# Kernel tuning notes

Measured on AMD Instinct MI355X. Metric: run time of the kernel, lower is better.

Reference implementation:

```python
import jax, jax.numpy as jnp
import numpy as np

H = 128; B = 128; NA = 32; N = B * NA; NH = 4; DH = H // NH; F = 2 * H + 3


def _ln(x, g, b, eps=1e-5):
    m = x.mean(-1, keepdims=True)
    v = ((x - m) ** 2).mean(-1, keepdims=True)
    return (x - m) / jnp.sqrt(v + eps) * g + b


def _silu(x):
    return x * jax.nn.sigmoid(x)


def setup_inputs() -> dict:
    key = jax.random.key(0)
    ks = jax.random.split(key, 16)
    def rn(i, shape, s=0.05):
        return jax.random.normal(ks[i], shape, jnp.float32) * s
    return dict(
        num_atoms=jnp.full((B,), NA, dtype=jnp.int32),
        elems=jax.random.randint(ks[0], (N,), 0, 119),
        cell=jnp.tile(10.0 * jnp.eye(3, dtype=jnp.float32), (B, 1)),  # [3B,3]
        coord=jax.random.uniform(ks[1], (N, 3), jnp.float32, 1.0, 9.0),
        emb=rn(2, (119, H), 1.0),
        ln_in_g=jnp.ones((H,), jnp.float32), ln_in_b=jnp.zeros((H,), jnp.float32),
        attn_in_w=rn(3, (H, 3 * H)), attn_in_b=jnp.zeros((3 * H,), jnp.float32),
        attn_out_w=rn(4, (H, H)), attn_out_b=jnp.zeros((H,), jnp.float32),
        ce_w1=rn(5, (3, H)), ce_b1=jnp.zeros((H,), jnp.float32),
        ce_w2=rn(6, (H, H)), ce_b2=jnp.zeros((H,), jnp.float32),
        ln_feat_g=jnp.ones((F,), jnp.float32), ln_feat_b=jnp.zeros((F,), jnp.float32),
        op_w1=rn(7, (F, H)), op_b1=jnp.zeros((H,), jnp.float32),
        op_ln1_g=jnp.ones((H,), jnp.float32), op_ln1_b=jnp.zeros((H,), jnp.float32),
        res_w1=rn(8, (H, H)), res_b1=jnp.zeros((H,), jnp.float32),
        res_ln_g=jnp.ones((H,), jnp.float32), res_ln_b=jnp.zeros((H,), jnp.float32),
        res_w2=rn(9, (H, H)), res_b2=jnp.zeros((H,), jnp.float32),
        op_ln2_g=jnp.ones((H,), jnp.float32), op_ln2_b=jnp.zeros((H,), jnp.float32),
        op_w3=rn(10, (H, 3)), op_b3=jnp.zeros((3,), jnp.float32),
    )


def reference(num_atoms, elems, cell, coord, emb, ln_in_g, ln_in_b,
              attn_in_w, attn_in_b, attn_out_w, attn_out_b,
              ce_w1, ce_b1, ce_w2, ce_b2, ln_feat_g, ln_feat_b,
              op_w1, op_b1, op_ln1_g, op_ln1_b,
              res_w1, res_b1, res_ln_g, res_ln_b, res_w2, res_b2,
              op_ln2_g, op_ln2_b, op_w3, op_b3):
    n = coord.shape[0]
    # atom embedding + input LayerNorm
    x = _ln(emb[elems], ln_in_g, ln_in_b)
    # unbatched multihead self-attention over all atoms (seq_len = n)
    qkv = x @ attn_in_w + attn_in_b
    q, k, v = jnp.split(qkv, 3, axis=-1)
    q = q.reshape(n, NH, DH); k = k.reshape(n, NH, DH); v = v.reshape(n, NH, DH)
    a = jax.nn.softmax(jnp.einsum('qhd,khd->hqk', q, k) / np.float32(np.sqrt(DH)), axis=-1)
    x = jnp.einsum('hqk,khd->qhd', a, v).reshape(n, H) @ attn_out_w + attn_out_b
    # cell encoder on [3B,3] rows
    cf = _silu(cell @ ce_w1 + ce_b1) @ ce_w2 + ce_b2
    bidx = jnp.repeat(jnp.arange(num_atoms.shape[0]), num_atoms, total_repeat_length=n)
    # torch: cf.repeat(B,1)[batch_idx] == cf[batch_idx] since batch_idx < B
    comb = _ln(jnp.concatenate([x, cf[bidx], coord], axis=-1), ln_feat_g, ln_feat_b)
    # offset predictor
    h = _silu(_ln(comb @ op_w1 + op_b1, op_ln1_g, op_ln1_b))
    h = h + (_silu(_ln(h @ res_w1 + res_b1, res_ln_g, res_ln_b)) @ res_w2 + res_b2)
    h = _ln(h, op_ln2_g, op_ln2_b)
    offset = jnp.tanh(h @ op_w3 + op_b3) * 0.01
    perturbed = coord + offset
    # per-molecule clamp: segment gather of per-cell-row min/max replaces the python loop
    c3 = cell.reshape(-1, 3, 3)           # [B,3,3]
    cmin = c3.min(axis=2) + 1e-6          # [B,3]
    cmax = c3.max(axis=2) - 1e-6          # [B,3]
    return jnp.clip(perturbed, cmin[bidx], cmax[bidx])
```

## Files before the change

### kernel.cpp

```cpp
#include <hip/hip_runtime.h>
#include <hip/hip_bf16.h>
#include <math.h>
#include <stdint.h>

#define NATOMS 4096
#define HD     128
#define NHEAD  4
#define DHEAD  32
#define FDIM   259
#define BATCH  128
#define H3X    384
#define SPLIT  4

typedef __attribute__((ext_vector_type(8))) short short8;
typedef __attribute__((ext_vector_type(4))) float float4v;
typedef __attribute__((ext_vector_type(16))) float f32x16;

__device__ __forceinline__ ushort f2bf(float f) {
    uint32_t u = __float_as_uint(f);
    return (ushort)((u + 0x7fffu + ((u >> 16) & 1u)) >> 16);
}
__device__ __forceinline__ float b2f(ushort u) {
    return __uint_as_float(((uint32_t)u) << 16);
}
__device__ __forceinline__ f32x16 z16() {
    f32x16 v;
#pragma unroll
    for (int i = 0; i < 16; i++) v[i] = 0.f;
    return v;
}

#define NB_PACK 528
#define NB_CELL 128
__global__ __launch_bounds__(256) void k_setup(
        const int* __restrict__ num_atoms, const float* __restrict__ cell,
        const float* __restrict__ qkvw, const float* __restrict__ aow,
        const float* __restrict__ op1w, const float* __restrict__ r1w,
        const float* __restrict__ r2w,
        const float* __restrict__ ce_w1, const float* __restrict__ ce_b1,
        const float* __restrict__ ce_w2, const float* __restrict__ ce_b2,
        int* __restrict__ bidx, float* __restrict__ cmin, float* __restrict__ cmax,
        ushort* __restrict__ Wqkv, ushort* __restrict__ Wao,
        ushort* __restrict__ Wop1, ushort* __restrict__ Wr1, ushort* __restrict__ Wr2,
        float* __restrict__ CF) {
    __shared__ float hs[HD];
    __shared__ int start[BATCH + 1];
    const int t = threadIdx.x;
    if (blockIdx.x < NB_PACK) {
        int idx = blockIdx.x * 256 + t;
        if (idx < 49152) {
            int n = idx >> 7, k = idx & 127;
            Wqkv[idx] = f2bf(qkvw[k * H3X + n]);
        } else if (idx < 65536) {
            int j = idx - 49152; int n = j >> 7, k = j & 127;
            Wao[j] = f2bf(aow[k * HD + n]);
        } else if (idx < 102400) {
            int j = idx - 65536; int n = j / 288, k = j - n * 288;
            Wop1[j] = (k < FDIM) ? f2bf(op1w[k * HD + n]) : (ushort)0;
        } else if (idx < 118784) {
            int j = idx - 102400; int n = j >> 7, k = j & 127;
            Wr1[j] = f2bf(r1w[k * HD + n]);
        } else if (idx < 135168) {
            int j = idx - 118784; int n = j >> 7, k = j & 127;
            Wr2[j] = f2bf(r2w[k * HD + n]);
        }
    } else if (blockIdx.x < NB_PACK + NB_CELL) {
        int r = blockIdx.x - NB_PACK;
        if (t < 128) {
            float c0 = cell[r * 3 + 0], c1 = cell[r * 3 + 1], c2 = cell[r * 3 + 2];
            float h = c0 * ce_w1[t] + c1 * ce_w1[HD + t] + c2 * ce_w1[2 * HD + t] + ce_b1[t];
            h = h / (1.f + __expf(-h));
            hs[t] = h;
        }
        __syncthreads();
        if (t < 128) {
            float acc = ce_b2[t];
#pragma unroll 8
            for (int k = 0; k < HD; k++) acc += hs[k] * ce_w2[k * HD + t];
            CF[r * HD + t] = acc;
        }
    } else {
        if (t == 0) {
            int pos = 0;
            for (int b = 0; b < BATCH; b++) { start[b] = pos; pos += num_atoms[b]; }
            start[BATCH] = pos;
        }
        __syncthreads();
        if (t < 128) {
            int s = min(start[t], NATOMS), e = min(start[t + 1], NATOMS);
            for (int j = s; j < e; j++) bidx[j] = t;
            if (t == 0) {
                int total = min(start[BATCH], NATOMS);
                for (int j = total; j < NATOMS; j++) bidx[j] = BATCH - 1;
            }
        }
        for (int rr = t; rr < BATCH * 3; rr += 256) {
            float a0 = cell[rr * 3 + 0], a1 = cell[rr * 3 + 1], a2 = cell[rr * 3 + 2];
            cmin[rr] = fminf(a0, fminf(a1, a2)) + 1e-6f;
            cmax[rr] = fmaxf(a0, fmaxf(a1, a2)) - 1e-6f;
        }
    }
}

__global__ __launch_bounds__(256) void k_qkv(const int* __restrict__ elems,
                                             const float* __restrict__ emb,
                                             const float* __restrict__ lg,
                                             const float* __restrict__ lb,
                                             const ushort* __restrict__ Wt,
                                             const float* __restrict__ bias,
                                             ushort* __restrict__ Qb, ushort* __restrict__ Kb,
                                             ushort* __restrict__ VTb2) {
    __shared__ alignas(16) ushort Af[4][64][8];
    __shared__ alignas(16) ushort vt[128][16];
    const int t = threadIdx.x, w = t >> 6, lane = t & 63, quad = lane >> 4, lq = lane & 15;
    const int rb = blockIdx.x * 16;
    {
        int row = t >> 4, seg = t & 15;
        int e = elems[rb + row];
        const float* ep = emb + (size_t)e * HD + seg * 8;
        float v[8]; float s = 0.f, ss = 0.f;
#pragma unroll
        for (int j = 0; j < 8; j++) { v[j] = ep[j]; s += v[j]; ss += v[j] * v[j]; }
#pragma unroll
        for (int m = 1; m < 16; m <<= 1) { s += __shfl_xor(s, m); ss += __shfl_xor(ss, m); }
        float mean = s * (1.f / HD);
        float inv = rsqrtf(ss * (1.f / HD) - mean * mean + 1e-5f);
        ushort o[8];
#pragma unroll
        for (int j = 0; j < 8; j++)
            o[j] = f2bf((v[j] - mean) * inv * lg[seg * 8 + j] + lb[seg * 8 + j]);
        *(uint4*)&Af[seg >> 2][(seg & 3) * 16 + row][0] = *(uint4*)o;
    }
    __syncthreads();
    float4v acc[6];
#pragma unroll
    for (int i = 0; i < 6; i++) acc[i] = (float4v){0.f, 0.f, 0.f, 0.f};
#pragma unroll
    for (int kt = 0; kt < 4; kt++) {
        short8 af = *(const short8*)&Af[kt][lane][0];
#pragma unroll
        for (int i = 0; i < 6; i++) {
            int nt = w * 6 + i;
            short8 wf = *(const short8*)(Wt + (size_t)(lq + 16 * nt) * HD + kt * 32 + quad * 8);
            acc[i] = __builtin_amdgcn_mfma_f32_16x16x32_bf16(af, wf, acc[i], 0, 0, 0);
        }
    }
#pragma unroll
    for (int i = 0; i < 6; i++) {
        int col = lq + 16 * (w * 6 + i);
        float bb = bias[col];
#pragma unroll
        for (int r = 0; r < 4; r++) {
            float c = acc[i][r] + bb;
            int rowin = quad * 4 + r;
            int row = rb + rowin;
            if (col < 128) {
                Qb[(size_t)(((col >> 5) * NATOMS) + row) * 32 + (col & 31)] = f2bf(c * 0.25503483f);
            } else if (col < 256) {
                int cc = col - 128;
                Kb[(size_t)(((cc >> 5) * NATOMS) + row) * 32 + (cc & 31)] = f2bf(c);
            } else {
                vt[col - 256][rowin] = f2bf(c);
            }
        }
    }
    __syncthreads();
    if (t < 128) {
        int hh = t >> 5, d = t & 31;
        uint4 a0 = *(const uint4*)&vt[t][0];
        uint4 a1 = *(const uint4*)&vt[t][8];
        ushort* dst = VTb2 + ((size_t)(hh * 64 + (rb >> 6)) * 32 + d) * 64 + (rb & 63);
        *(uint4*)(dst) = a0;
        *(uint4*)(dst + 8) = a1;
    }
}

__global__ __launch_bounds__(256) void k_attn(const ushort* __restrict__ Qb,
                                              const ushort* __restrict__ Kb,
                                              const ushort* __restrict__ VTb2,
                                              ushort* __restrict__ Opart,
                                              float* __restrict__ lpart) {
    __shared__ alignas(16) ushort P_s[4][32 * 72];
    __shared__ alignas(16) float OL[2][32 * 36];
    __shared__ float LL[2][32];
    const int t = threadIdx.x, w = t >> 6, lane = t & 63;
    const int l31 = lane & 31, hi = lane >> 5;
    const int qt = w & 1, kh2 = w >> 1;
    const int h = blockIdx.y, sp = blockIdx.z;
    const int q0 = blockIdx.x * 64;
    const int qrow = q0 + qt * 32 + l31;

    short8 qf0 = *(const short8*)(Qb + (size_t)(h * NATOMS + qrow) * 32 + hi * 8);
    short8 qf1 = *(const short8*)(Qb + (size_t)(h * NATOMS + qrow) * 32 + 16 + hi * 8);
    f32x16 O = z16();
    float lp = 0.f;
    ushort* Pw = &P_s[w][0];
    const int kstart = sp * (NATOMS / SPLIT) + kh2 * 64;

    for (int ck = 0; ck < (NATOMS / SPLIT) / 128; ck++) {
        int kb = kstart + ck * 128;
        const ushort* vbase = VTb2 + ((size_t)(h * 64 + (kb >> 6)) * 32 + l31) * 64;
#pragma unroll
        for (int kt = 0; kt < 2; kt++) {
            int kk = kb + kt * 32;
            const ushort* kp = Kb + (size_t)(h * NATOMS + kk + l31) * 32 + hi * 8;
            short8 kf0 = *(const short8*)(kp);
            short8 kf1 = *(const short8*)(kp + 16);
            f32x16 S = z16();
            S = __builtin_amdgcn_mfma_f32_32x32x16_bf16(kf0, qf0, S, 0, 0, 0);
            S = __builtin_amdgcn_mfma_f32_32x32x16_bf16(kf1, qf1, S, 0, 0, 0);
#pragma unroll
            for (int c = 0; c < 4; c++) {
                float p0 = exp2f(S[4 * c + 0]);
                float p1 = exp2f(S[4 * c + 1]);
                float p2 = exp2f(S[4 * c + 2]);
                float p3 = exp2f(S[4 * c + 3]);
                lp += (p0 + p1) + (p2 + p3);
                uint32_t u0 = __float_as_uint(p0) + 0x8000u;
                uint32_t u1 = __float_as_uint(p1) + 0x8000u;
                uint32_t u2 = __float_as_uint(p2) + 0x8000u;
                uint32_t u3 = __float_as_uint(p3) + 0x8000u;
                uint2 u;
                u.x = __builtin_amdgcn_perm(u1, u0, 0x07060302u);
                u.y = __builtin_amdgcn_perm(u3, u2, 0x07060302u);
                *(uint2*)(&Pw[l31 * 72 + kt * 32 + c * 8 + hi * 4]) = u;
            }
#pragma unroll
            for (int wd = 0; wd < 2; wd++) {
                int koff = kt * 32 + wd * 16;
                short8 vf = *(const short8*)(vbase + koff + hi * 8);
                short8 pf = *(const short8*)(&Pw[l31 * 72 + koff + hi * 8]);
                O = __builtin_amdgcn_mfma_f32_32x32x16_bf16(vf, pf, O, 0, 0, 0);
            }
        }
    }
    lp += __shfl_xor(lp, 32);
    if (kh2 == 0) {
#pragma unroll
        for (int c = 0; c < 4; c++) {
            float4 f = {O[4 * c + 0], O[4 * c + 1], O[4 * c + 2], O[4 * c + 3]};
            *(float4*)(&OL[qt][l31 * 36 + c * 8 + hi * 4]) = f;
        }
        if (hi == 0) LL[qt][l31] = lp;
    }
    __syncthreads();
    if (kh2 == 1) {
        lp += LL[qt][l31];
#pragma unroll
        for (int c = 0; c < 4; c++) {
            float4 f = *(const float4*)(&OL[qt][l31 * 36 + c * 8 + hi * 4]);
            float o0 = O[4 * c + 0] + f.x, o1 = O[4 * c + 1] + f.y;
            float o2 = O[4 * c + 2] + f.z, o3 = O[4 * c + 3] + f.w;
            uint2 u;
            u.x = (uint32_t)f2bf(o0) | ((uint32_t)f2bf(o1) << 16);
            u.y = (uint32_t)f2bf(o2) | ((uint32_t)f2bf(o3) << 16);
            *(uint2*)(Opart + (size_t)(sp * NATOMS + qrow) * HD + h * 32 + c * 8 + hi * 4) = u;
        }
        if (hi == 0) lpart[sp * (NHEAD * NATOMS) + h * NATOMS + qrow] = lp;
    }
}

__global__ __launch_bounds__(256) void k_back(
        const ushort* __restrict__ Opart, const float* __restrict__ lpart,
        const ushort* __restrict__ Wao, const float* __restrict__ aob,
        const float* __restrict__ CF, const float* __restrict__ coord,
        const int* __restrict__ bidx,
        const float* __restrict__ fg, const float* __restrict__ fb,
        const ushort* __restrict__ Wop1, const float* __restrict__ op1b,
        const float* __restrict__ l1g, const float* __restrict__ l1b,
        const ushort* __restrict__ Wr1, const float* __restrict__ r1b,
        const float* __restrict__ rlg, const float* __restrict__ rlb,
        const ushort* __restrict__ Wr2, const float* __restrict__ r2b,
        const float* __restrict__ l2g, const float* __restrict__ l2b,
        const float* __restrict__ w3, const float* __restrict__ b3,
        const float* __restrict__ cmin, const float* __restrict__ cmax,
        float* __restrict__ out) {
    __shared__ alignas(16) ushort AF1[9][64][8];
    __shared__ alignas(16) ushort AF2[4][64][8];
    __shared__ alignas(16) ushort AF3[4][64][8];
    __shared__ float RED[4][16][4];
    __shared__ float REDC[16][2];
    __shared__ float COORDS[16][3];
    const int t = threadIdx.x, w = t >> 6, lane = t & 63, quad = lane >> 4, lq = lane & 15;
    const int rb = blockIdx.x * 16;
    const int col0 = lq + 32 * w, col1 = col0 + 16;

    const int arow = rb + lq;
    float4v a0 = {0.f,0.f,0.f,0.f}, a1 = {0.f,0.f,0.f,0.f};
#pragma unroll
    for (int h = 0; h < 4; h++) {
        float l = 0.f;
#pragma unroll
        for (int s = 0; s < SPLIT; s++) l += lpart[s * (NHEAD * NATOMS) + h * NATOMS + arow];
        float inv = 1.f / l;
        float pv[8];
#pragma unroll
        for (int j = 0; j < 8; j++) pv[j] = 0.f;
#pragma unroll
        for (int s = 0; s < SPLIT; s++) {
            short8 ov = *(const short8*)(Opart + (size_t)(s * NATOMS + arow) * HD + h * 32 + quad * 8);
#pragma unroll
            for (int j = 0; j < 8; j++) pv[j] += b2f((ushort)ov[j]);
        }
        short8 af;
#pragma unroll
        for (int j = 0; j < 8; j++) af[j] = (short)f2bf(pv[j] * inv);
        short8 w0 = *(const short8*)(Wao + (size_t)col0 * HD + h * 32 + quad * 8);
        short8 w1 = *(const short8*)(Wao + (size_t)col1 * HD + h * 32 + quad * 8);
        a0 = __builtin_amdgcn_mfma_f32_16x16x32_bf16(af, w0, a0, 0, 0, 0);
        a1 = __builtin_amdgcn_mfma_f32_16x16x32_bf16(af, w1, a1, 0, 0, 0);
    }
    float x1[2][4];
#pragma unroll
    for (int r = 0; r < 4; r++) { x1[0][r] = a0[r] + aob[col0]; x1[1][r] = a1[r] + aob[col1]; }

    float cfv[2][4];
#pragma unroll
    for (int r = 0; r < 4; r++) {
        int bi = bidx[rb + quad * 4 + r];
        cfv[0][r] = CF[bi * HD + col0];
        cfv[1][r] = CF[bi * HD + col1];
    }
#pragma unroll
    for (int r = 0; r < 4; r++) {
        float s1 = x1[0][r] + x1[1][r] + cfv[0][r] + cfv[1][r];
        float s2 = x1[0][r]*x1[0][r] + x1[1][r]*x1[1][r] + cfv[0][r]*cfv[0][r] + cfv[1][r]*cfv[1][r];
#pragma unroll
        for (int m = 1; m < 16; m <<= 1) { s1 += __shfl_xor(s1, m); s2 += __shfl_xor(s2, m); }
        if (lq == 0) { RED[w][quad * 4 + r][0] = s1; RED[w][quad * 4 + r][1] = s2; }
    }
    if (t < 16) {
        float c0 = coord[(rb + t) * 3 + 0], c1 = coord[(rb + t) * 3 + 1], c2 = coord[(rb + t) * 3 + 2];
        COORDS[t][0] = c0; COORDS[t][1] = c1; COORDS[t][2] = c2;
        REDC[t][0] = c0 + c1 + c2; REDC[t][1] = c0*c0 + c1*c1 + c2*c2;
    }
    if (t < 64) { uint4 z = {0,0,0,0}; *(uint4*)&AF1[8][t][0] = z; }
    __syncthreads();
    {
#pragma unroll
        for (int r = 0; r < 4; r++) {
            int ri = quad * 4 + r;
            float s1 = RED[0][ri][0] + RED[1][ri][0] + RED[2][ri][0] + RED[3][ri][0] + REDC[ri][0];
            float s2 = RED[0][ri][1] + RED[1][ri][1] + RED[2][ri][1] + RED[3][ri][1] + REDC[ri][1];
            float mn = s1 * (1.f / FDIM);
            float iv = rsqrtf(s2 * (1.f / FDIM) - mn * mn + 1e-5f);
#pragma unroll
            for (int i = 0; i < 2; i++) {
                int c = i ? col1 : col0;
                float vx = ((i ? x1[1][r] : x1[0][r]) - mn) * iv * fg[c] + fb[c];
                float vc = ((i ? cfv[1][r] : cfv[0][r]) - mn) * iv * fg[c + 128] + fb[c + 128];
                AF1[c >> 5][((c >> 3) & 3) * 16 + ri][c & 7] = f2bf(vx);
                int c2 = c + 128;
                AF1[c2 >> 5][((c2 >> 3) & 3) * 16 + ri][c2 & 7] = f2bf(vc);
            }
        }
        if (t < 16) {
            float s1 = RED[0][t][0] + RED[1][t][0] + RED[2][t][0] + RED[3][t][0] + REDC[t][0];
            float s2 = RED[0][t][1] + RED[1][t][1] + RED[2][t][1] + RED[3][t][1] + REDC[t][1];
            float mn = s1 * (1.f / FDIM);
            float iv = rsqrtf(s2 * (1.f / FDIM) - mn * mn + 1e-5f);
#pragma unroll
            for (int c = 0; c < 3; c++)
                AF1[8][t][c] = f2bf((COORDS[t][c] - mn) * iv * fg[256 + c] + fb[256 + c]);
        }
    }
    __syncthreads();

    float4v c0v = {0.f,0.f,0.f,0.f}, c1v = {0.f,0.f,0.f,0.f};
#pragma unroll
    for (int kt = 0; kt < 9; kt++) {
        short8 af = *(const short8*)&AF1[kt][lane][0];
        short8 w0 = *(const short8*)(Wop1 + (size_t)col0 * 288 + kt * 32 + quad * 8);
        short8 w1 = *(const short8*)(Wop1 + (size_t)col1 * 288 + kt * 32 + quad * 8);
        c0v = __builtin_amdgcn_mfma_f32_16x16x32_bf16(af, w0, c0v, 0, 0, 0);
        c1v = __builtin_amdgcn_mfma_f32_16x16x32_bf16(af, w1, c1v, 0, 0, 0);
    }
    float h0[4], h1[4];
#pragma unroll
    for (int r = 0; r < 4; r++) {
        h0[r] = c0v[r] + op1b[col0]; h1[r] = c1v[r] + op1b[col1];
        float s1 = h0[r] + h1[r], s2 = h0[r]*h0[r] + h1[r]*h1[r];
#pragma unroll
        for (int m = 1; m < 16; m <<= 1) { s1 += __shfl_xor(s1, m); s2 += __shfl_xor(s2, m); }
        if (lq == 0) { RED[w][quad * 4 + r][0] = s1; RED[w][quad * 4 + r][1] = s2; }
    }
    __syncthreads();
#pragma unroll
    for (int r = 0; r < 4; r++) {
        int ri = quad * 4 + r;
        float s1 = RED[0][ri][0] + RED[1][ri][0] + RED[2][ri][0] + RED[3][ri][0];
        float s2 = RED[0][ri][1] + RED[1][ri][1] + RED[2][ri][1] + RED[3][ri][1];
        float mn = s1 * (1.f / HD);
        float iv = rsqrtf(s2 * (1.f / HD) - mn * mn + 1e-5f);
#pragma unroll
        for (int i = 0; i < 2; i++) {
            int c = i ? col1 : col0;
            float o = ((i ? h1[r] : h0[r]) - mn) * iv * l1g[c] + l1b[c];
            o = o / (1.f + __expf(-o));
            AF2[c >> 5][((c >> 3) & 3) * 16 + ri][c & 7] = f2bf(o);
        }
    }
    __syncthreads();

    float4v d0v = {0.f,0.f,0.f,0.f}, d1v = {0.f,0.f,0.f,0.f};
#pragma unroll
    for (int kt = 0; kt < 4; kt++) {
        short8 af = *(const short8*)&AF2[kt][lane][0];
        short8 w0 = *(const short8*)(Wr1 + (size_t)col0 * HD + kt * 32 + quad * 8);
        short8 w1 = *(const short8*)(Wr1 + (size_t)col1 * HD + kt * 32 + quad * 8);
        d0v = __builtin_amdgcn_mfma_f32_16x16x32_bf16(af, w0, d0v, 0, 0, 0);
        d1v = __builtin_amdgcn_mfma_f32_16x16x32_bf16(af, w1, d1v, 0, 0, 0);
    }
    float e0[4], e1[4];
#pragma unroll
    for (int r = 0; r < 4; r++) {
        e0[r] = d0v[r] + r1b[col0]; e1[r] = d1v[r] + r1b[col1];
        float s1 = e0[r] + e1[r], s2 = e0[r]*e0[r] + e1[r]*e1[r];
#pragma unroll
        for (int m = 1; m < 16; m <<= 1) { s1 += __shfl_xor(s1, m); s2 += __shfl_xor(s2, m); }
        if (lq == 0) { RED[w][quad * 4 + r][0] = s1; RED[w][quad * 4 + r][1] = s2; }
    }
    __syncthreads();
#pragma unroll
    for (int r = 0; r < 4; r++) {
        int ri = quad * 4 + r;
        float s1 = RED[0][ri][0] + RED[1][ri][0] + RED[2][ri][0] + RED[3][ri][0];
        float s2 = RED[0][ri][1] + RED[1][ri][1] + RED[2][ri][1] + RED[3][ri][1];
        float mn = s1 * (1.f / HD);
        float iv = rsqrtf(s2 * (1.f / HD) - mn * mn + 1e-5f);
#pragma unroll
        for (int i = 0; i < 2; i++) {
            int c = i ? col1 : col0;
            float o = ((i ? e1[r] : e0[r]) - mn) * iv * rlg[c] + rlb[c];
            o = o / (1.f + __expf(-o));
            AF3[c >> 5][((c >> 3) & 3) * 16 + ri][c & 7] = f2bf(o);
        }
    }
    __syncthreads();

    float4v f0v = {0.f,0.f,0.f,0.f}, f1v = {0.f,0.f,0.f,0.f};
#pragma unroll
    for (int kt = 0; kt < 4; kt++) {
        short8 af = *(const short8*)&AF3[kt][lane][0];
        short8 w0 = *(const short8*)(Wr2 + (size_t)col0 * HD + kt * 32 + quad * 8);
        short8 w1 = *(const short8*)(Wr2 + (size_t)col1 * HD + kt * 32 + quad * 8);
        f0v = __builtin_amdgcn_mfma_f32_16x16x32_bf16(af, w0, f0v, 0, 0, 0);
        f1v = __builtin_amdgcn_mfma_f32_16x16x32_bf16(af, w1, f1v, 0, 0, 0);
    }
    float g0r[4], g1r[4];
#pragma unroll
    for (int r = 0; r < 4; r++) {
        int ri = quad * 4 + r;
        float rs0 = b2f(AF2[col0 >> 5][((col0 >> 3) & 3) * 16 + ri][col0 & 7]);
        float rs1 = b2f(AF2[col1 >> 5][((col1 >> 3) & 3) * 16 + ri][col1 & 7]);
        g0r[r] = f0v[r] + r2b[col0] + rs0;
        g1r[r] = f1v[r] + r2b[col1] + rs1;
        float s1 = g0r[r] + g1r[r], s2 = g0r[r]*g0r[r] + g1r[r]*g1r[r];
#pragma unroll
        for (int m = 1; m < 16; m <<= 1) { s1 += __shfl_xor(s1, m); s2 += __shfl_xor(s2, m); }
        if (lq == 0) { RED[w][ri][0] = s1; RED[w][ri][1] = s2; }
    }
    __syncthreads();
    float tp[4][3];
#pragma unroll
    for (int r = 0; r < 4; r++) {
        int ri = quad * 4 + r;
        float s1 = RED[0][ri][0] + RED[1][ri][0] + RED[2][ri][0] + RED[3][ri][0];
        float s2 = RED[0][ri][1] + RED[1][ri][1] + RED[2][ri][1] + RED[3][ri][1];
        float mn = s1 * (1.f / HD);
        float iv = rsqrtf(s2 * (1.f / HD) - mn * mn + 1e-5f);
        float h20 = (g0r[r] - mn) * iv * l2g[col0] + l2b[col0];
        float h21 = (g1r[r] - mn) * iv * l2g[col1] + l2b[col1];
#pragma unroll
        for (int c = 0; c < 3; c++) {
            float v = h20 * w3[col0 * 3 + c] + h21 * w3[col1 * 3 + c];
#pragma unroll
            for (int m = 1; m < 16; m <<= 1) v += __shfl_xor(v, m);
            tp[r][c] = v;
        }
    }
    __syncthreads();
    if (lq == 0) {
#pragma unroll
        for (int r = 0; r < 4; r++) {
            RED[w][quad * 4 + r][0] = tp[r][0];
            RED[w][quad * 4 + r][1] = tp[r][1];
            RED[w][quad * 4 + r][2] = tp[r][2];
        }
    }
    __syncthreads();
    if (t < 16) {
        int bi = bidx[rb + t];
#pragma unroll
        for (int c = 0; c < 3; c++) {
            float sv = RED[0][t][c] + RED[1][t][c] + RED[2][t][c] + RED[3][t][c];
            float off = tanhf(sv + b3[c]) * 0.01f;
            float pert = COORDS[t][c] + off;
            pert = fminf(fmaxf(pert, cmin[bi * 3 + c]), cmax[bi * 3 + c]);
            out[(rb + t) * 3 + c] = pert;
        }
    }
}

extern "C" void kernel_launch(void* const* d_in, const int* in_sizes, int n_in,
                              void* d_out, int out_size, void* d_ws, size_t ws_size,
                              hipStream_t stream) {
    const int* num_atoms = (const int*)d_in[0];
    const int* elems = (const int*)d_in[1];
    const float* cell = (const float*)d_in[2];
    const float* coord = (const float*)d_in[3];
    const float* emb = (const float*)d_in[4];
    const float* ln_in_g = (const float*)d_in[5];
    const float* ln_in_b = (const float*)d_in[6];
    const float* attn_in_w = (const float*)d_in[7];
    const float* attn_in_b = (const float*)d_in[8];
    const float* attn_out_w = (const float*)d_in[9];
    const float* attn_out_b = (const float*)d_in[10];
    const float* ce_w1 = (const float*)d_in[11];
    const float* ce_b1 = (const float*)d_in[12];
    const float* ce_w2 = (const float*)d_in[13];
    const float* ce_b2 = (const float*)d_in[14];
    const float* ln_feat_g = (const float*)d_in[15];
    const float* ln_feat_b = (const float*)d_in[16];
    const float* op_w1 = (const float*)d_in[17];
    const float* op_b1 = (const float*)d_in[18];
    const float* op_ln1_g = (const float*)d_in[19];
    const float* op_ln1_b = (const float*)d_in[20];
    const float* res_w1 = (const float*)d_in[21];
    const float* res_b1 = (const float*)d_in[22];
    const float* res_ln_g = (const float*)d_in[23];
    const float* res_ln_b = (const float*)d_in[24];
    const float* res_w2 = (const float*)d_in[25];
    const float* res_b2 = (const float*)d_in[26];
    const float* op_ln2_g = (const float*)d_in[27];
    const float* op_ln2_b = (const float*)d_in[28];
    const float* op_w3 = (const float*)d_in[29];
    const float* op_b3 = (const float*)d_in[30];

    char* ws = (char*)d_ws;
    const size_t MB = 1u << 20;
    ushort* Qb = (ushort*)(ws);
    ushort* Kb = (ushort*)(ws + 1 * MB);
    ushort* VTb2 = (ushort*)(ws + 2 * MB);
    ushort* Opart = (ushort*)(ws + 3 * MB);
    float* lpart = (float*)(ws + 7 * MB);
    int* bidx = (int*)(ws + 7 * MB + (256u << 10));
    float* cmin = (float*)(ws + 7 * MB + (272u << 10));
    float* cmax = (float*)(ws + 7 * MB + (274u << 10));
    float* CF = (float*)(ws + 7 * MB + (276u << 10));
    ushort* Wqkv = (ushort*)(ws + 7 * MB + (340u << 10));
    ushort* Wao = (ushort*)(ws + 7 * MB + (436u << 10));
    ushort* Wop1 = (ushort*)(ws + 7 * MB + (468u << 10));
    ushort* Wr1 = (ushort*)(ws + 7 * MB + (540u << 10));
    ushort* Wr2 = (ushort*)(ws + 7 * MB + (572u << 10));

    k_setup<<<NB_PACK + NB_CELL + 1, 256, 0, stream>>>(
        num_atoms, cell, attn_in_w, attn_out_w, op_w1, res_w1, res_w2,
        ce_w1, ce_b1, ce_w2, ce_b2,
        bidx, cmin, cmax, Wqkv, Wao, Wop1, Wr1, Wr2, CF);
    k_qkv<<<256, 256, 0, stream>>>(elems, emb, ln_in_g, ln_in_b, Wqkv, attn_in_b,
                                   Qb, Kb, VTb2);
    k_attn<<<dim3(NATOMS / 64, NHEAD, SPLIT), 256, 0, stream>>>(Qb, Kb, VTb2, Opart, lpart);
    k_back<<<256, 256, 0, stream>>>(Opart, lpart, Wao, attn_out_b, CF, coord, bidx,
                                    ln_feat_g, ln_feat_b, Wop1, op_b1, op_ln1_g, op_ln1_b,
                                    Wr1, res_b1, res_ln_g, res_ln_b, Wr2, res_b2,
                                    op_ln2_g, op_ln2_b, op_w3, op_b3, cmin, cmax,
                                    (float*)d_out);
}
```

Measured before the change: 179.4 us.

## Widen k_back to 8 waves, one column tile each; coalesce weight-pack reads

k_back now launches 512 threads (8 waves), and each wave computes a single 16-column MFMA tile instead of two, so the per-wave serial chain of MFMAs and LayerNorm work is halved. Cross-wave reductions grow from 4 to 8 partial sums per row. Separately, the weight-packing setup kernel now reads source weights in row order and scatters the transposed bf16 writes, making global reads coalesced while writes become strided. The trade is more threads and larger reductions per block against shorter per-wave dependency chains in a kernel with only 256 blocks.

```diff
diff --git a/kernel.cpp b/kernel.cpp
--- a/kernel.cpp
+++ b/kernel.cpp
@@ -49,20 +49,23 @@
     if (blockIdx.x < NB_PACK) {
         int idx = blockIdx.x * 256 + t;
         if (idx < 49152) {
-            int n = idx >> 7, k = idx & 127;
-            Wqkv[idx] = f2bf(qkvw[k * H3X + n]);
+            int k = idx / 384, n = idx - k * 384;
+            Wqkv[n * 128 + k] = f2bf(qkvw[idx]);
         } else if (idx < 65536) {
-            int j = idx - 49152; int n = j >> 7, k = j & 127;
-            Wao[j] = f2bf(aow[k * HD + n]);
+            int j = idx - 49152; int k = j >> 7, n = j & 127;
+            Wao[n * 128 + k] = f2bf(aow[j]);
+        } else if (idx < 98688) {
+            int j = idx - 65536; int k = j >> 7, n = j & 127;
+            Wop1[n * 288 + k] = f2bf(op1w[j]);
         } else if (idx < 102400) {
-            int j = idx - 65536; int n = j / 288, k = j - n * 288;
-            Wop1[j] = (k < FDIM) ? f2bf(op1w[k * HD + n]) : (ushort)0;
+            int j = idx - 98688; int n = j & 127, k = 259 + (j >> 7);
+            Wop1[n * 288 + k] = 0;
         } else if (idx < 118784) {
-            int j = idx - 102400; int n = j >> 7, k = j & 127;
-            Wr1[j] = f2bf(r1w[k * HD + n]);
-        } else if (idx < 135168) {
-            int j = idx - 118784; int n = j >> 7, k = j & 127;
-            Wr2[j] = f2bf(r2w[k * HD + n]);
+            int j = idx - 102400; int k = j >> 7, n = j & 127;
+            Wr1[n * 128 + k] = f2bf(r1w[j]);
+        } else {
+            int j = idx - 118784; int k = j >> 7, n = j & 127;
+            Wr2[n * 128 + k] = f2bf(r2w[j]);
         }
     } else if (blockIdx.x < NB_PACK + NB_CELL) {
         int r = blockIdx.x - NB_PACK;
@@ -260,7 +263,7 @@
     }
 }
 
-__global__ __launch_bounds__(256) void k_back(
+__global__ __launch_bounds__(512) void k_back(
         const ushort* __restrict__ Opart, const float* __restrict__ lpart,
         const ushort* __restrict__ Wao, const float* __restrict__ aob,
         const float* __restrict__ CF, const float* __restrict__ coord,
@@ -278,15 +281,15 @@
     __shared__ alignas(16) ushort AF1[9][64][8];
     __shared__ alignas(16) ushort AF2[4][64][8];
     __shared__ alignas(16) ushort AF3[4][64][8];
-    __shared__ float RED[4][16][4];
+    __shared__ float RED[8][16][4];
     __shared__ float REDC[16][2];
     __shared__ float COORDS[16][3];
     const int t = threadIdx.x, w = t >> 6, lane = t & 63, quad = lane >> 4, lq = lane & 15;
     const int rb = blockIdx.x * 16;
-    const int col0 = lq + 32 * w, col1 = col0 + 16;
+    const int col = lq + 16 * w;
 
     const int arow = rb + lq;
-    float4v a0 = {0.f,0.f,0.f,0.f}, a1 = {0.f,0.f,0.f,0.f};
+    float4v a0 = {0.f, 0.f, 0.f, 0.f};
 #pragma unroll
     for (int h = 0; h < 4; h++) {
         float l = 0.f;
@@ -305,26 +308,20 @@
         short8 af;
 #pragma unroll
         for (int j = 0; j < 8; j++) af[j] = (short)f2bf(pv[j] * inv);
-        short8 w0 = *(const short8*)(Wao + (size_t)col0 * HD + h * 32 + quad * 8);
-        short8 w1 = *(const short8*)(Wao + (size_t)col1 * HD + h * 32 + quad * 8);
+        short8 w0 = *(const short8*)(Wao + (size_t)col * HD + h * 32 + quad * 8);
         a0 = __builtin_amdgcn_mfma_f32_16x16x32_bf16(af, w0, a0, 0, 0, 0);
-        a1 = __builtin_amdgcn_mfma_f32_16x16x32_bf16(af, w1, a1, 0, 0, 0);
-    }
-    float x1[2][4];
-#pragma unroll
-    for (int r = 0; r < 4; r++) { x1[0][r] = a0[r] + aob[col0]; x1[1][r] = a1[r] + aob[col1]; }
-
-    float cfv[2][4];
-#pragma unroll
-    for (int r = 0; r < 4; r++) {
-        int bi = bidx[rb + quad * 4 + r];
-        cfv[0][r] = CF[bi * HD + col0];
-        cfv[1][r] = CF[bi * HD + col1];
-    }
-#pragma unroll
-    for (int r = 0; r < 4; r++) {
-        float s1 = x1[0][r] + x1[1][r] + cfv[0][r] + cfv[1][r];
-        float s2 = x1[0][r]*x1[0][r] + x1[1][r]*x1[1][r] + cfv[0][r]*cfv[0][r] + cfv[1][r]*cfv[1][r];
+    }
+    float x1[4];
+#pragma unroll
+    for (int r = 0; r < 4; r++) x1[r] = a0[r] + aob[col];
+
+    float cfv[4];
+#pragma unroll
+    for (int r = 0; r < 4; r++) cfv[r] = CF[bidx[rb + quad * 4 + r] * HD + col];
+#pragma unroll
+    for (int r = 0; r < 4; r++) {
+        float s1 = x1[r] + cfv[r];
+        float s2 = x1[r] * x1[r] + cfv[r] * cfv[r];
 #pragma unroll
         for (int m = 1; m < 16; m <<= 1) { s1 += __shfl_xor(s1, m); s2 += __shfl_xor(s2, m); }
         if (lq == 0) { RED[w][quad * 4 + r][0] = s1; RED[w][quad * 4 + r][1] = s2; }
@@ -332,54 +329,48 @@
     if (t < 16) {
         float c0 = coord[(rb + t) * 3 + 0], c1 = coord[(rb + t) * 3 + 1], c2 = coord[(rb + t) * 3 + 2];
         COORDS[t][0] = c0; COORDS[t][1] = c1; COORDS[t][2] = c2;
-        REDC[t][0] = c0 + c1 + c2; REDC[t][1] = c0*c0 + c1*c1 + c2*c2;
-    }
-    if (t < 64) { uint4 z = {0,0,0,0}; *(uint4*)&AF1[8][t][0] = z; }
-    __syncthreads();
-    {
-#pragma unroll
-        for (int r = 0; r < 4; r++) {
-            int ri = quad * 4 + r;
-            float s1 = RED[0][ri][0] + RED[1][ri][0] + RED[2][ri][0] + RED[3][ri][0] + REDC[ri][0];
-            float s2 = RED[0][ri][1] + RED[1][ri][1] + RED[2][ri][1] + RED[3][ri][1] + REDC[ri][1];
-            float mn = s1 * (1.f / FDIM);
-            float iv = rsqrtf(s2 * (1.f / FDIM) - mn * mn + 1e-5f);
-#pragma unroll
-            for (int i = 0; i < 2; i++) {
-                int c = i ? col1 : col0;
-                float vx = ((i ? x1[1][r] : x1[0][r]) - mn) * iv * fg[c] + fb[c];
-                float vc = ((i ? cfv[1][r] : cfv[0][r]) - mn) * iv * fg[c + 128] + fb[c + 128];
-                AF1[c >> 5][((c >> 3) & 3) * 16 + ri][c & 7] = f2bf(vx);
-                int c2 = c + 128;
-                AF1[c2 >> 5][((c2 >> 3) & 3) * 16 + ri][c2 & 7] = f2bf(vc);
-            }
-        }
-        if (t < 16) {
-            float s1 = RED[0][t][0] + RED[1][t][0] + RED[2][t][0] + RED[3][t][0] + REDC[t][0];
-            float s2 = RED[0][t][1] + RED[1][t][1] + RED[2][t][1] + RED[3][t][1] + REDC[t][1];
-            float mn = s1 * (1.f / FDIM);
-            float iv = rsqrtf(s2 * (1.f / FDIM) - mn * mn + 1e-5f);
-#pragma unroll
-            for (int c = 0; c < 3; c++)
-                AF1[8][t][c] = f2bf((COORDS[t][c] - mn) * iv * fg[256 + c] + fb[256 + c]);
-        }
-    }
-    __syncthreads();
-
-    float4v c0v = {0.f,0.f,0.f,0.f}, c1v = {0.f,0.f,0.f,0.f};
+        REDC[t][0] = c0 + c1 + c2; REDC[t][1] = c0 * c0 + c1 * c1 + c2 * c2;
+    }
+    if (t < 64) { uint4 z = {0, 0, 0, 0}; *(uint4*)&AF1[8][t][0] = z; }
+    __syncthreads();
+#pragma unroll
+    for (int r = 0; r < 4; r++) {
+        int ri = quad * 4 + r;
+        float s1 = REDC[ri][0], s2 = REDC[ri][1];
+#pragma unroll
+        for (int ww = 0; ww < 8; ww++) { s1 += RED[ww][ri][0]; s2 += RED[ww][ri][1]; }
+        float mn = s1 * (1.f / FDIM);
+        float iv = rsqrtf(s2 * (1.f / FDIM) - mn * mn + 1e-5f);
+        float vx = (x1[r] - mn) * iv * fg[col] + fb[col];
+        float vc = (cfv[r] - mn) * iv * fg[col + 128] + fb[col + 128];
+        AF1[col >> 5][((col >> 3) & 3) * 16 + ri][col & 7] = f2bf(vx);
+        int c2 = col + 128;
+        AF1[c2 >> 5][((c2 >> 3) & 3) * 16 + ri][c2 & 7] = f2bf(vc);
+    }
+    if (t < 16) {
+        float s1 = REDC[t][0], s2 = REDC[t][1];
+#pragma unroll
+        for (int ww = 0; ww < 8; ww++) { s1 += RED[ww][t][0]; s2 += RED[ww][t][1]; }
+        float mn = s1 * (1.f / FDIM);
+        float iv = rsqrtf(s2 * (1.f / FDIM) - mn * mn + 1e-5f);
+#pragma unroll
+        for (int c = 0; c < 3; c++)
+            AF1[8][t][c] = f2bf((COORDS[t][c] - mn) * iv * fg[256 + c] + fb[256 + c]);
+    }
+    __syncthreads();
+
+    float4v cv = {0.f, 0.f, 0.f, 0.f};
 #pragma unroll
     for (int kt = 0; kt < 9; kt++) {
         short8 af = *(const short8*)&AF1[kt][lane][0];
-        short8 w0 = *(const short8*)(Wop1 + (size_t)col0 * 288 + kt * 32 + quad * 8);
-        short8 w1 = *(const short8*)(Wop1 + (size_t)col1 * 288 + kt * 32 + quad * 8);
-        c0v = __builtin_amdgcn_mfma_f32_16x16x32_bf16(af, w0, c0v, 0, 0, 0);
-        c1v = __builtin_amdgcn_mfma_f32_16x16x32_bf16(af, w1, c1v, 0, 0, 0);
-    }
-    float h0[4], h1[4];
-#pragma unroll
-    for (int r = 0; r < 4; r++) {
-        h0[r] = c0v[r] + op1b[col0]; h1[r] = c1v[r] + op1b[col1];
-        float s1 = h0[r] + h1[r], s2 = h0[r]*h0[r] + h1[r]*h1[r];
+        short8 w0 = *(const short8*)(Wop1 + (size_t)col * 288 + kt * 32 + quad * 8);
+        cv = __builtin_amdgcn_mfma_f32_16x16x32_bf16(af, w0, cv, 0, 0, 0);
+    }
+    float h0[4];
+#pragma unroll
+    for (int r = 0; r < 4; r++) {
+        h0[r] = cv[r] + op1b[col];
+        float s1 = h0[r], s2 = h0[r] * h0[r];
 #pragma unroll
         for (int m = 1; m < 16; m <<= 1) { s1 += __shfl_xor(s1, m); s2 += __shfl_xor(s2, m); }
         if (lq == 0) { RED[w][quad * 4 + r][0] = s1; RED[w][quad * 4 + r][1] = s2; }
@@ -388,34 +379,29 @@
 #pragma unroll
     for (int r = 0; r < 4; r++) {
         int ri = quad * 4 + r;
-        float s1 = RED[0][ri][0] + RED[1][ri][0] + RED[2][ri][0] + RED[3][ri][0];
-        float s2 = RED[0][ri][1] + RED[1][ri][1] + RED[2][ri][1] + RED[3][ri][1];
+        float s1 = 0.f, s2 = 0.f;
+#pragma unroll
+        for (int ww = 0; ww < 8; ww++) { s1 += RED[ww][ri][0]; s2 += RED[ww][ri][1]; }
         float mn = s1 * (1.f / HD);
         float iv = rsqrtf(s2 * (1.f / HD) - mn * mn + 1e-5f);
-#pragma unroll
-        for (int i = 0; i < 2; i++) {
-            int c = i ? col1 : col0;
-            float o = ((i ? h1[r] : h0[r]) - mn) * iv * l1g[c] + l1b[c];
-            o = o / (1.f + __expf(-o));
-            AF2[c >> 5][((c >> 3) & 3) * 16 + ri][c & 7] = f2bf(o);
-        }
-    }
-    __syncthreads();
-
-    float4v d0v = {0.f,0.f,0.f,0.f}, d1v = {0.f,0.f,0.f,0.f};
+        float o = (h0[r] - mn) * iv * l1g[col] + l1b[col];
+        o = o / (1.f + __expf(-o));
+        AF2[col >> 5][((col >> 3) & 3) * 16 + ri][col & 7] = f2bf(o);
+    }
+    __syncthreads();
+
+    float4v dv = {0.f, 0.f, 0.f, 0.f};
 #pragma unroll
     for (int kt = 0; kt < 4; kt++) {
         short8 af = *(const short8*)&AF2[kt][lane][0];
-        short8 w0 = *(const short8*)(Wr1 + (size_t)col0 * HD + kt * 32 + quad * 8);
-        short8 w1 = *(const short8*)(Wr1 + (size_t)col1 * HD + kt * 32 + quad * 8);
-        d0v = __builtin_amdgcn_mfma_f32_16x16x32_bf16(af, w0, d0v, 0, 0, 0);
-        d1v = __builtin_amdgcn_mfma_f32_16x16x32_bf16(af, w1, d1v, 0, 0, 0);
-    }
-    float e0[4], e1[4];
-#pragma unroll
-    for (int r = 0; r < 4; r++) {
-        e0[r] = d0v[r] + r1b[col0]; e1[r] = d1v[r] + r1b[col1];
-        float s1 = e0[r] + e1[r], s2 = e0[r]*e0[r] + e1[r]*e1[r];
+        short8 w0 = *(const short8*)(Wr1 + (size_t)col * HD + kt * 32 + quad * 8);
+        dv = __builtin_amdgcn_mfma_f32_16x16x32_bf16(af, w0, dv, 0, 0, 0);
+    }
+    float e0[4];
+#pragma unroll
+    for (int r = 0; r < 4; r++) {
+        e0[r] = dv[r] + r1b[col];
+        float s1 = e0[r], s2 = e0[r] * e0[r];
 #pragma unroll
         for (int m = 1; m < 16; m <<= 1) { s1 += __shfl_xor(s1, m); s2 += __shfl_xor(s2, m); }
         if (lq == 0) { RED[w][quad * 4 + r][0] = s1; RED[w][quad * 4 + r][1] = s2; }
@@ -424,38 +410,31 @@
 #pragma unroll
     for (int r = 0; r < 4; r++) {
         int ri = quad * 4 + r;
-        float s1 = RED[0][ri][0] + RED[1][ri][0] + RED[2][ri][0] + RED[3][ri][0];
-        float s2 = RED[0][ri][1] + RED[1][ri][1] + RED[2][ri][1] + RED[3][ri][1];
+        float s1 = 0.f, s2 = 0.f;
+#pragma unroll
+        for (int ww = 0; ww < 8; ww++) { s1 += RED[ww][ri][0]; s2 += RED[ww][ri][1]; }
         float mn = s1 * (1.f / HD);
         float iv = rsqrtf(s2 * (1.f / HD) - mn * mn + 1e-5f);
-#pragma unroll
-        for (int i = 0; i < 2; i++) {
-            int c = i ? col1 : col0;
-            float o = ((i ? e1[r] : e0[r]) - mn) * iv * rlg[c] + rlb[c];
-            o = o / (1.f + __expf(-o));
-            AF3[c >> 5][((c >> 3) & 3) * 16 + ri][c & 7] = f2bf(o);
-        }
-    }
-    __syncthreads();
-
-    float4v f0v = {0.f,0.f,0.f,0.f}, f1v = {0.f,0.f,0.f,0.f};
+        float o = (e0[r] - mn) * iv * rlg[col] + rlb[col];
+        o = o / (1.f + __expf(-o));
+        AF3[col >> 5][((col >> 3) & 3) * 16 + ri][col & 7] = f2bf(o);
+    }
+    __syncthreads();
+
+    float4v fv = {0.f, 0.f, 0.f, 0.f};
 #pragma unroll
     for (int kt = 0; kt < 4; kt++) {
         short8 af = *(const short8*)&AF3[kt][lane][0];
-        short8 w0 = *(const short8*)(Wr2 + (size_t)col0 * HD + kt * 32 + quad * 8);
-        short8 w1 = *(const short8*)(Wr2 + (size_t)col1 * HD + kt * 32 + quad * 8);
-        f0v = __builtin_amdgcn_mfma_f32_16x16x32_bf16(af, w0, f0v, 0, 0, 0);
-        f1v = __builtin_amdgcn_mfma_f32_16x16x32_bf16(af, w1, f1v, 0, 0, 0);
-    }
-    float g0r[4], g1r[4];
+        short8 w0 = *(const short8*)(Wr2 + (size_t)col * HD + kt * 32 + quad * 8);
+        fv = __builtin_amdgcn_mfma_f32_16x16x32_bf16(af, w0, fv, 0, 0, 0);
+    }
+    float g0r[4];
 #pragma unroll
     for (int r = 0; r < 4; r++) {
         int ri = quad * 4 + r;
-        float rs0 = b2f(AF2[col0 >> 5][((col0 >> 3) & 3) * 16 + ri][col0 & 7]);
-        float rs1 = b2f(AF2[col1 >> 5][((col1 >> 3) & 3) * 16 + ri][col1 & 7]);
-        g0r[r] = f0v[r] + r2b[col0] + rs0;
-        g1r[r] = f1v[r] + r2b[col1] + rs1;
-        float s1 = g0r[r] + g1r[r], s2 = g0r[r]*g0r[r] + g1r[r]*g1r[r];
+        float rs = b2f(AF2[col >> 5][((col >> 3) & 3) * 16 + ri][col & 7]);
+        g0r[r] = fv[r] + r2b[col] + rs;
+        float s1 = g0r[r], s2 = g0r[r] * g0r[r];
 #pragma unroll
         for (int m = 1; m < 16; m <<= 1) { s1 += __shfl_xor(s1, m); s2 += __shfl_xor(s2, m); }
         if (lq == 0) { RED[w][ri][0] = s1; RED[w][ri][1] = s2; }
@@ -465,15 +444,15 @@
 #pragma unroll
     for (int r = 0; r < 4; r++) {
         int ri = quad * 4 + r;
-        float s1 = RED[0][ri][0] + RED[1][ri][0] + RED[2][ri][0] + RED[3][ri][0];
-        float s2 = RED[0][ri][1] + RED[1][ri][1] + RED[2][ri][1] + RED[3][ri][1];
+        float s1 = 0.f, s2 = 0.f;
+#pragma unroll
+        for (int ww = 0; ww < 8; ww++) { s1 += RED[ww][ri][0]; s2 += RED[ww][ri][1]; }
         float mn = s1 * (1.f / HD);
         float iv = rsqrtf(s2 * (1.f / HD) - mn * mn + 1e-5f);
-        float h20 = (g0r[r] - mn) * iv * l2g[col0] + l2b[col0];
-        float h21 = (g1r[r] - mn) * iv * l2g[col1] + l2b[col1];
+        float h2 = (g0r[r] - mn) * iv * l2g[col] + l2b[col];
 #pragma unroll
         for (int c = 0; c < 3; c++) {
-            float v = h20 * w3[col0 * 3 + c] + h21 * w3[col1 * 3 + c];
+            float v = h2 * w3[col * 3 + c];
 #pragma unroll
             for (int m = 1; m < 16; m <<= 1) v += __shfl_xor(v, m);
             tp[r][c] = v;
@@ -493,7 +472,9 @@
         int bi = bidx[rb + t];
 #pragma unroll
         for (int c = 0; c < 3; c++) {
-            float sv = RED[0][t][c] + RED[1][t][c] + RED[2][t][c] + RED[3][t][c];
+            float sv = 0.f;
+#pragma unroll
+            for (int ww = 0; ww < 8; ww++) sv += RED[ww][t][c];
             float off = tanhf(sv + b3[c]) * 0.01f;
             float pert = COORDS[t][c] + off;
             pert = fminf(fmaxf(pert, cmin[bi * 3 + c]), cmax[bi * 3 + c]);
@@ -561,7 +542,7 @@
     k_qkv<<<256, 256, 0, stream>>>(elems, emb, ln_in_g, ln_in_b, Wqkv, attn_in_b,
                                    Qb, Kb, VTb2);
     k_attn<<<dim3(NATOMS / 64, NHEAD, SPLIT), 256, 0, stream>>>(Qb, Kb, VTb2, Opart, lpart);
-    k_back<<<256, 256, 0, stream>>>(Opart, lpart, Wao, attn_out_b, CF, coord, bidx,
+    k_back<<<256, 512, 0, stream>>>(Opart, lpart, Wao, attn_out_b, CF, coord, bidx,
                                     ln_feat_g, ln_feat_b, Wop1, op_b1, op_ln1_g, op_ln1_b,
                                     Wr1, res_b1, res_ln_g, res_ln_b, Wr2, res_b2,
                                     op_ln2_g, op_ln2_b, op_w3, op_b3, cmin, cmax,
```

Result: no change. 177.2 us (-1.2%).
